# Kernel tuning notes

Hardware: AMD Instinct MI355X
Metric: run time of the kernel (lower is better)

Reference implementation:

```python
import jax, jax.numpy as jnp
import numpy as np

BS, D = 4096, 128
NUM_CLASSES = 512
K = 4          # opt.pk
MARGIN = 0.1   # opt.margin
NEG = -1e30    # sentinel for masked-out entries (finite to avoid inf*0 NaNs)


def setup_inputs() -> dict:
    key = jax.random.key(0)
    k1, k2 = jax.random.split(key)
    batch_reprs = jax.random.normal(k1, (BS, D), dtype=jnp.float32)
    batch_labels = jax.random.randint(k2, (BS,), 0, NUM_CLASSES, dtype=jnp.int64)
    return {"batch_reprs": batch_reprs, "batch_labels": batch_labels}


def _pairwise_dist(x, eps=1e-16):
    # Euclidean distance matrix, squared=False, with the usual zero-distance
    # masking trick for sqrt differentiability (as in the source repo's dist()).
    prod = x @ x.T                              # [B,B]
    sq = jnp.diagonal(prod)                     # [B]
    d2 = jnp.maximum(sq[:, None] + sq[None, :] - 2.0 * prod, 0.0)
    zero_mask = (d2 == 0.0).astype(x.dtype)
    d = jnp.sqrt(d2 + zero_mask * eps)
    return d * (1.0 - zero_mask)


def reference(batch_reprs, batch_labels):
    # class-match matrix: 1 where same class (includes self-match on diagonal)
    cls_match = (batch_labels[:, None] == batch_labels[None, :]).astype(jnp.float32)  # [B,B]

    sim_mat = -_pairwise_dist(batch_reprs)                      # use_similarity=False path
    simi_hat = sim_mat + (1.0 - cls_match) * MARGIN             # margin-shifted similarities

    # rank positions (1-based) under descending sort of simi_hat, per row
    orgp = jnp.argsort(-simi_hat, axis=1)                       # descending order indices
    rank = jnp.argsort(orgp, axis=1) + 1                        # [B,B] int ranks

    pos_nums = jnp.sum(cls_match, axis=1).astype(jnp.int32)     # n_+ per row (incl. self)
    ks = jnp.minimum(pos_nums, K + 1)                           # clamp(max=k+1)

    fp_mask = (cls_match < 1.0) & (rank <= ks[:, None])         # false positives in top-k
    fp_nums = jnp.sum(fp_mask, axis=1)                          # |N| per row, int
    fn_mask = (cls_match > 0.0) & (rank > ks[:, None])          # false negatives beyond k

    # per-row top-|N| of false-negative similarities, vectorized over rows
    fn_vals = jnp.where(fn_mask, simi_hat, NEG)
    fn_sorted = -jnp.sort(-fn_vals, axis=1)                     # descending
    col = jnp.arange(simi_hat.shape[1])[None, :]
    top_fn_sum = jnp.sum(jnp.where(col < fp_nums[:, None], fn_sorted, 0.0), axis=1)

    fp_sum = jnp.sum(jnp.where(fp_mask, simi_hat, 0.0), axis=1)

    # rows with fp_num == 0 contribute 0 in both terms, matching the python loop
    return jnp.sum(fp_sum - top_fn_sum)
```

## Files before the change

### kernel.cpp

```cpp
#include <hip/hip_runtime.h>
#include <math.h>

#define BS 4096
#define D 128
#define NS 32
#define SC 128
#define MARGINF 0.1f
#define NEGV -1e30f
#define BIGD 1e30f
#define LSTR 12

typedef float f32x4 __attribute__((ext_vector_type(4)));
typedef short s16x8 __attribute__((ext_vector_type(8)));

#define GLD_LDS16(gsrc, ldst) __builtin_amdgcn_global_load_lds( \
    (const __attribute__((address_space(1))) unsigned int*)(const void*)(gsrc), \
    (__attribute__((address_space(3))) unsigned int*)(void*)(ldst), 16, 0, 0)

__device__ __forceinline__ unsigned short f2bf(float f) {
    unsigned int u = __float_as_uint(f);
    unsigned int r = u + 0x7FFFu + ((u >> 16) & 1u);
    return (unsigned short)(r >> 16);
}

__device__ __forceinline__ void insV(float v, float (&V)[5]) {
    float w0 = fminf(V[0], v);
    float w1 = __builtin_amdgcn_fmed3f(V[0], V[1], v);
    float w2 = __builtin_amdgcn_fmed3f(V[1], V[2], v);
    float w3 = __builtin_amdgcn_fmed3f(V[2], V[3], v);
    float w4 = __builtin_amdgcn_fmed3f(V[3], V[4], v);
    V[0] = w0; V[1] = w1; V[2] = w2; V[3] = w3; V[4] = w4;
}

__device__ __forceinline__ void insDF(float v, int f, float (&V)[5], int (&F)[5]) {
#pragma unroll
    for (int t = 0; t < 5; ++t) {
        bool c = v > V[t];
        float tv = V[t]; int tf = F[t];
        V[t] = c ? v : tv; F[t] = c ? f : tf;
        v = c ? tv : v;    f = c ? tf : f;
    }
}

__global__ __launch_bounds__(256) void prep_kernel(
        const float* __restrict__ X, float* __restrict__ norms,
        unsigned short* __restrict__ Xp, int* __restrict__ ticket) {
    __shared__ __align__(16) unsigned short sb[32 * 128];
    const int t = threadIdx.x, bx = blockIdx.x;
    const int row0 = bx * 32;

    if (bx == 0 && t == 0) ticket[0] = 0;

#pragma unroll
    for (int i = 0; i < 4; ++i) {
        int idx = i * 256 + t;
        int lr = idx >> 5, kq = idx & 31;
        float4 v = ((const float4*)X)[(size_t)row0 * 32 + idx];
        float acc = v.x * v.x + v.y * v.y + v.z * v.z + v.w * v.w;
#pragma unroll
        for (int off = 1; off < 32; off <<= 1) acc += __shfl_xor(acc, off);
        if (kq == 0) norms[row0 + lr] = acc;
        ushort4 hv = { f2bf(v.x), f2bf(v.y), f2bf(v.z), f2bf(v.w) };
        int chunk = (kq >> 1) ^ (lr & 7);
        *(ushort4*)((char*)sb + lr * 256 + (chunk << 4) + (kq & 1) * 8) = hv;
    }
    __syncthreads();

#pragma unroll
    for (int i = 0; i < 2; ++i) {
        int u = i * 256 + t;
        int j = u >> 8, ug = u & 255;
        int ks = ug >> 6, l2 = ug & 63;
        int lr = j * 16 + (l2 & 15), q = l2 >> 4;
        int chunk = (ks * 4 + q) ^ (lr & 7);
        ulonglong2 d = *(const ulonglong2*)((const char*)sb + lr * 256 + (chunk << 4));
        *(ulonglong2*)((char*)Xp + (size_t)(bx * 2 + j) * 4096 + ks * 1024 + l2 * 16) = d;
    }
}

__global__ __launch_bounds__(256, 5) void main_kernel(
        const unsigned short* __restrict__ Xp, const int* __restrict__ labels,
        const float* __restrict__ norms, float* __restrict__ lists) {
    __shared__ __align__(16) char shA[32768];
    const int t = threadIdx.x, bx = blockIdx.x;
    const int slice = bx & (NS - 1);
    const int col0 = slice * SC;
    const int w = t >> 6, l = t & 63, rl = l & 15, q = l >> 4;
    const int gRow = (bx >> 5) * 4 + w;
    const int rowG = gRow * 16 + rl;
    const int lR = labels[rowG];
    const char* Pb = (const char*)Xp;

#pragma unroll
    for (int c = 0; c < 8; ++c) {
        int chunk = w * 8 + c;
        const char* src = Pb + (size_t)(slice * 8 + (chunk >> 2)) * 4096
                             + (chunk & 3) * 1024 + l * 16;
        GLD_LDS16(src, shA + chunk * 1024);
    }

    s16x8 brow[4];
#pragma unroll
    for (int ks = 0; ks < 4; ++ks)
        brow[ks] = *(const s16x8*)(Pb + (size_t)gRow * 4096 + ks * 1024 + l * 16);

    __syncthreads();

    f32x4 acc[8];
#pragma unroll
    for (int i = 0; i < 8; ++i) acc[i] = (f32x4){0.f, 0.f, 0.f, 0.f};

#pragma unroll
    for (int ks = 0; ks < 4; ++ks) {
        s16x8 af[8];
#pragma unroll
        for (int i = 0; i < 8; ++i)
            af[i] = *(const s16x8*)(shA + i * 4096 + ks * 1024 + l * 16);
#pragma unroll
        for (int i = 0; i < 8; ++i)
            acc[i] = __builtin_amdgcn_mfma_f32_16x16x32_bf16(af[i], brow[ks], acc[i], 0, 0, 0);
    }

    float dV[5], sV[5];
#pragma unroll
    for (int i = 0; i < 5; ++i) { dV[i] = BIGD; sV[i] = BIGD; }
    int cnt = 0;

#pragma unroll
    for (int i = 0; i < 8; ++i) {
        f32x4 nc4 = *(const f32x4*)(norms + col0 + i * 16 + q * 4);
        int4  lc4 = *(const int4*)(labels + col0 + i * 16 + q * 4);
        int lcv[4] = {lc4.x, lc4.y, lc4.z, lc4.w};
#pragma unroll
        for (int e = 0; e < 4; ++e) {
            float v = fmaf(acc[i][e], -2.f, nc4[e]);
            bool same = (lcv[e] == lR);
            cnt += same ? 1 : 0;
            insV(same ? BIGD : v, dV);
            if (__any(same)) insV(same ? v : BIGD, sV);
        }
    }

#pragma unroll
    for (int off = 16; off <= 32; off <<= 1) {
        float bv[5];
#pragma unroll
        for (int i = 0; i < 5; ++i) bv[i] = __shfl_xor(dV[i], off);
#pragma unroll
        for (int i = 0; i < 5; ++i) insV(bv[i], dV);
#pragma unroll
        for (int i = 0; i < 5; ++i) bv[i] = __shfl_xor(sV[i], off);
#pragma unroll
        for (int i = 0; i < 5; ++i) insV(bv[i], sV);
        cnt += __shfl_xor(cnt, off);
    }

    if (q == 0) {
        float* Lp = lists + ((size_t)rowG * NS + slice) * LSTR;
        *(f32x4*)Lp       = (f32x4){dV[0], dV[1], dV[2], dV[3]};
        *(f32x4*)(Lp + 4) = (f32x4){dV[4], sV[4], (float)cnt, 0.f};
        *(f32x4*)(Lp + 8) = (f32x4){sV[0], sV[1], sV[2], sV[3]};
    }
}

__global__ __launch_bounds__(256) void merge_kernel(
        const float* __restrict__ lists, const int* __restrict__ labels,
        const float* __restrict__ norms, float* __restrict__ partials,
        int* __restrict__ ticket, float* __restrict__ out) {
    __shared__ float sh[256];
    __shared__ int lastFlag;
    const int t = threadIdx.x, bx = blockIdx.x;
    const int gid = bx * 256 + t;
    const int r = gid >> 4, part = gid & 15;

    float dV[5], sV[5];
#pragma unroll
    for (int i = 0; i < 5; ++i) { dV[i] = BIGD; sV[i] = BIGD; }
    float cntf = 0.f;
#pragma unroll
    for (int s = 0; s < 2; ++s) {
        const float* rec = lists + (size_t)(r * NS + part * 2 + s) * LSTR;
        f32x4 a = *(const f32x4*)rec;
        f32x4 b = *(const f32x4*)(rec + 4);
        f32x4 c = *(const f32x4*)(rec + 8);
        insV(a.x, dV); insV(a.y, dV); insV(a.z, dV); insV(a.w, dV); insV(b.x, dV);
        insV(c.x, sV); insV(c.y, sV); insV(c.z, sV); insV(c.w, sV); insV(b.y, sV);
        cntf += b.z;
    }

#pragma unroll
    for (int off = 1; off <= 8; off <<= 1) {
        float bv[5];
#pragma unroll
        for (int i = 0; i < 5; ++i) bv[i] = __shfl_xor(dV[i], off);
#pragma unroll
        for (int i = 0; i < 5; ++i) insV(bv[i], dV);
#pragma unroll
        for (int i = 0; i < 5; ++i) bv[i] = __shfl_xor(sV[i], off);
#pragma unroll
        for (int i = 0; i < 5; ++i) insV(bv[i], sV);
        cntf += __shfl_xor(cntf, off);
    }

    float res = 0.f;
    if (part == 0) {
        const float nR = norms[r];
        const int pos = (int)cntf;
        const int ks = (pos < 5) ? pos : 5;
        float dS[5], sS[5];
#pragma unroll
        for (int i = 0; i < 5; ++i) {
            float dv = dV[i]; bool ok = dv < 1e29f;
            dS[i] = ok ? (-sqrtf(fmaxf(nR + dv, 0.f)) + MARGINF) : NEGV;
        }
#pragma unroll
        for (int i = 0; i < 5; ++i) {
            float sv = sV[i]; bool ok = sv < 1e29f;
            sS[i] = ok ? -sqrtf(fmaxf(nR + sv, 0.f)) : NEGV;
        }
        float mV[5]; int mF[5];
#pragma unroll
        for (int i = 0; i < 5; ++i) { mV[i] = dS[i]; mF[i] = 0; }
#pragma unroll
        for (int i = 0; i < 5; ++i) insDF(sS[i], 1, mV, mF);

        float fpsum = 0.f; int fpn = 0;
#pragma unroll
        for (int i = 0; i < 5; ++i)
            if (i < ks && mF[i] == 0) { fpsum += mV[i]; fpn++; }
        const int s0 = ks - fpn;
        float fnsum = 0.f;
#pragma unroll
        for (int i = 0; i < 5; ++i)
            if (i >= s0 && i < s0 + fpn) fnsum += sS[i];
        res = fpsum - fnsum;
    }
    sh[t] = res;
    __syncthreads();
    for (int s = 128; s > 0; s >>= 1) {
        if (t < s) sh[t] += sh[t + s];
        __syncthreads();
    }
    if (t == 0) {
        partials[bx] = sh[0];
        __threadfence();
        int old = atomicAdd(ticket, 1);
        lastFlag = (old == (int)gridDim.x - 1) ? 1 : 0;
    }
    __syncthreads();
    if (lastFlag) {
        __threadfence();
        sh[t] = partials[t];
        __syncthreads();
        for (int s = 128; s > 0; s >>= 1) {
            if (t < s) sh[t] += sh[t + s];
            __syncthreads();
        }
        if (t == 0) out[0] = sh[0];
    }
}

extern "C" void kernel_launch(void* const* d_in, const int* in_sizes, int n_in,
                              void* d_out, int out_size, void* d_ws, size_t ws_size,
                              hipStream_t stream) {
    const float* X      = (const float*)d_in[0];
    const int*   labels = (const int*)d_in[1];

    float* ws       = (float*)d_ws;
    float* norms    = ws;
    float* partials = ws + BS;
    int*   ticket   = (int*)(ws + BS + 256);
    float* lists    = ws + BS + 256 + 16;
    unsigned short* Xp = (unsigned short*)(lists + (size_t)BS * NS * LSTR);

    prep_kernel<<<BS / 32, 256, 0, stream>>>(X, norms, Xp, ticket);
    main_kernel<<<(BS / 64) * NS, 256, 0, stream>>>(Xp, labels, norms, lists);
    merge_kernel<<<(BS * 16) / 256, 256, 0, stream>>>(lists, labels, norms,
                                                      partials, ticket, (float*)d_out);
}
```

Measured before the change: 39.21 us.

## Fuse prep into main kernel, converting fp32 to bf16 in-block

Removes the separate prep kernel. Each main-kernel block now reads its 128-column slice and its 64 rows straight from the fp32 input, computes norms and bf16 conversion itself, and writes the MFMA-ready layout into LDS. This saves one kernel launch and the round trip through the packed bf16 buffer. In exchange every block redundantly converts data that 64 row-blocks share, reads twice the bytes in fp32, and the occupancy hint drops from 5 to 4 blocks per CU. The merge kernel still reads norms, which only the rp==0 blocks write, so correctness relies on kernel ordering.

```diff
diff --git a/kernel.cpp b/kernel.cpp
--- a/kernel.cpp
+++ b/kernel.cpp
@@ -13,10 +13,6 @@
 typedef float f32x4 __attribute__((ext_vector_type(4)));
 typedef short s16x8 __attribute__((ext_vector_type(8)));
 
-#define GLD_LDS16(gsrc, ldst) __builtin_amdgcn_global_load_lds( \
-    (const __attribute__((address_space(1))) unsigned int*)(const void*)(gsrc), \
-    (__attribute__((address_space(3))) unsigned int*)(void*)(ldst), 16, 0, 0)
-
 __device__ __forceinline__ unsigned short f2bf(float f) {
     unsigned int u = __float_as_uint(f);
     unsigned int r = u + 0x7FFFu + ((u >> 16) & 1u);
@@ -42,67 +38,54 @@
     }
 }
 
-__global__ __launch_bounds__(256) void prep_kernel(
-        const float* __restrict__ X, float* __restrict__ norms,
-        unsigned short* __restrict__ Xp, int* __restrict__ ticket) {
-    __shared__ __align__(16) unsigned short sb[32 * 128];
-    const int t = threadIdx.x, bx = blockIdx.x;
-    const int row0 = bx * 32;
-
-    if (bx == 0 && t == 0) ticket[0] = 0;
-
-#pragma unroll
-    for (int i = 0; i < 4; ++i) {
-        int idx = i * 256 + t;
-        int lr = idx >> 5, kq = idx & 31;
-        float4 v = ((const float4*)X)[(size_t)row0 * 32 + idx];
-        float acc = v.x * v.x + v.y * v.y + v.z * v.z + v.w * v.w;
-#pragma unroll
-        for (int off = 1; off < 32; off <<= 1) acc += __shfl_xor(acc, off);
-        if (kq == 0) norms[row0 + lr] = acc;
-        ushort4 hv = { f2bf(v.x), f2bf(v.y), f2bf(v.z), f2bf(v.w) };
-        int chunk = (kq >> 1) ^ (lr & 7);
-        *(ushort4*)((char*)sb + lr * 256 + (chunk << 4) + (kq & 1) * 8) = hv;
-    }
-    __syncthreads();
-
-#pragma unroll
-    for (int i = 0; i < 2; ++i) {
-        int u = i * 256 + t;
-        int j = u >> 8, ug = u & 255;
-        int ks = ug >> 6, l2 = ug & 63;
-        int lr = j * 16 + (l2 & 15), q = l2 >> 4;
-        int chunk = (ks * 4 + q) ^ (lr & 7);
-        ulonglong2 d = *(const ulonglong2*)((const char*)sb + lr * 256 + (chunk << 4));
-        *(ulonglong2*)((char*)Xp + (size_t)(bx * 2 + j) * 4096 + ks * 1024 + l2 * 16) = d;
-    }
-}
-
-__global__ __launch_bounds__(256, 5) void main_kernel(
-        const unsigned short* __restrict__ Xp, const int* __restrict__ labels,
-        const float* __restrict__ norms, float* __restrict__ lists) {
+__global__ __launch_bounds__(256, 4) void main_kernel(
+        const float* __restrict__ X, const int* __restrict__ labels,
+        float* __restrict__ norms, float* __restrict__ lists,
+        int* __restrict__ ticket) {
     __shared__ __align__(16) char shA[32768];
+    __shared__ float ncS[128];
     const int t = threadIdx.x, bx = blockIdx.x;
     const int slice = bx & (NS - 1);
     const int col0 = slice * SC;
+    const int rp = bx >> 5;
     const int w = t >> 6, l = t & 63, rl = l & 15, q = l >> 4;
-    const int gRow = (bx >> 5) * 4 + w;
+    const int gRow = rp * 4 + w;
     const int rowG = gRow * 16 + rl;
     const int lR = labels[rowG];
-    const char* Pb = (const char*)Xp;
-
-#pragma unroll
-    for (int c = 0; c < 8; ++c) {
-        int chunk = w * 8 + c;
-        const char* src = Pb + (size_t)(slice * 8 + (chunk >> 2)) * 4096
-                             + (chunk & 3) * 1024 + l * 16;
-        GLD_LDS16(src, shA + chunk * 1024);
+
+    if (bx == 0 && t == 0) ticket[0] = 0;
+
+#pragma unroll
+    for (int i = 0; i < 16; ++i) {
+        int idx = i * 256 + t;
+        int c = idx >> 5, kq = idx & 31;
+        float4 v = ((const float4*)X)[(size_t)(col0 + c) * 32 + kq];
+        float acc = v.x * v.x + v.y * v.y + v.z * v.z + v.w * v.w;
+#pragma unroll
+        for (int off = 1; off < 32; off <<= 1) acc += __shfl_xor(acc, off);
+        if (kq == 0) {
+            ncS[c] = acc;
+            if (rp == 0) norms[col0 + c] = acc;
+        }
+        ushort4 hv = { f2bf(v.x), f2bf(v.y), f2bf(v.z), f2bf(v.w) };
+        int cg = c >> 4, crl = c & 15;
+        int ks = kq >> 3, cq = (kq >> 1) & 3, half = kq & 1;
+        *(ushort4*)(shA + cg * 4096 + ks * 1024 + (cq * 16 + crl) * 16 + half * 8) = hv;
     }
 
     s16x8 brow[4];
 #pragma unroll
-    for (int ks = 0; ks < 4; ++ks)
-        brow[ks] = *(const s16x8*)(Pb + (size_t)gRow * 4096 + ks * 1024 + l * 16);
+    for (int ks = 0; ks < 4; ++ks) {
+        const float* rp8 = X + (size_t)rowG * D + ks * 32 + q * 8;
+        float4 v0 = *(const float4*)rp8;
+        float4 v1 = *(const float4*)(rp8 + 4);
+        s16x8 b;
+        b[0] = (short)f2bf(v0.x); b[1] = (short)f2bf(v0.y);
+        b[2] = (short)f2bf(v0.z); b[3] = (short)f2bf(v0.w);
+        b[4] = (short)f2bf(v1.x); b[5] = (short)f2bf(v1.y);
+        b[6] = (short)f2bf(v1.z); b[7] = (short)f2bf(v1.w);
+        brow[ks] = b;
+    }
 
     __syncthreads();
 
@@ -128,7 +111,7 @@
 
 #pragma unroll
     for (int i = 0; i < 8; ++i) {
-        f32x4 nc4 = *(const f32x4*)(norms + col0 + i * 16 + q * 4);
+        f32x4 nc4 = *(const f32x4*)&ncS[i * 16 + q * 4];
         int4  lc4 = *(const int4*)(labels + col0 + i * 16 + q * 4);
         int lcv[4] = {lc4.x, lc4.y, lc4.z, lc4.w};
 #pragma unroll
@@ -271,10 +254,8 @@
     float* partials = ws + BS;
     int*   ticket   = (int*)(ws + BS + 256);
     float* lists    = ws + BS + 256 + 16;
-    unsigned short* Xp = (unsigned short*)(lists + (size_t)BS * NS * LSTR);
-
-    prep_kernel<<<BS / 32, 256, 0, stream>>>(X, norms, Xp, ticket);
-    main_kernel<<<(BS / 64) * NS, 256, 0, stream>>>(Xp, labels, norms, lists);
+
+    main_kernel<<<(BS / 64) * NS, 256, 0, stream>>>(X, labels, norms, lists, ticket);
     merge_kernel<<<(BS * 16) / 256, 256, 0, stream>>>(lists, labels, norms,
                                                       partials, ticket, (float*)d_out);
 }
```

Result: slower. 49.48 us (+26.2%).
